# Performance work log

Hardware: AMD Instinct MI355X
Metric: run time of the kernel (lower is better)

Reference implementation:

```python
import jax, jax.numpy as jnp
import numpy as np

BATCH_SIZE = 512
NUM_ID = 64
FEAT_DIMS = 512
GROUP = BATCH_SIZE // NUM_ID


def setup_inputs() -> dict:
    key = jax.random.key(0)
    k1, k2 = jax.random.split(key)
    f_s = jax.random.normal(k1, (BATCH_SIZE, FEAT_DIMS), dtype=jnp.float32)
    f_t = jax.random.normal(k2, (BATCH_SIZE, FEAT_DIMS), dtype=jnp.float32)
    return {"f_s": f_s, "f_t": f_t}


def reference(f_s, f_t):
    B, g, n_id = BATCH_SIZE, GROUP, NUM_ID
    # all-pairs similarity: (B, B)
    sim_all = f_s @ f_t.T
    # sim_diff[i, j, k] = sim_all[i, k] - sim_all[i, j]  -> (B, B, B)
    sim_diff = sim_all[:, None, :] - sim_all[:, :, None]
    mask = 1.0 - jnp.eye(B, dtype=sim_all.dtype)  # over (j, k)
    sim_sg = jax.nn.relu(sim_diff) * mask[None, :, :]
    sim_all_rk = jnp.sum(sim_sg, axis=-1) + 1.0  # (B, B)

    # per-class positive similarities
    xs = f_s.reshape(n_id, g, FEAT_DIMS)
    xt = f_t.reshape(n_id, g, FEAT_DIMS)
    sim_pos = jnp.einsum('nid,njd->nij', xs, xt)  # (n_id, g, g)
    # sim_pos_diff[n, i, j, k] = sim_pos[n, i, k] - sim_pos[n, i, j]
    sim_pos_diff = sim_pos[:, :, None, :] - sim_pos[:, :, :, None]
    pos_mask = 1.0 - jnp.eye(g, dtype=sim_pos.dtype)  # over (j, k)
    sim_pos_sg = jax.nn.relu(sim_pos_diff) * pos_mask[None, None, :, :]
    sim_pos_rk = jnp.sum(sim_pos_sg, axis=-1) + 1.0  # (n_id, g, g)

    # block-diagonal (per-id) slices of sim_all_rk: (n_id, g, g)
    blocks = sim_all_rk.reshape(n_id, g, n_id, g)
    idx = jnp.arange(n_id)
    diag_blocks = blocks[idx, :, idx, :]  # (n_id, g, g)

    ap = jnp.sum(sim_pos_rk / diag_blocks) / g / B
    return 1.0 - ap
```

## Files before the change

### kernel.cpp

```cpp
#include <hip/hip_runtime.h>

typedef __attribute__((ext_vector_type(8))) short bf16x8;
typedef __attribute__((ext_vector_type(4))) float f32x4;

#define NB 512
#define FD 512
#define PLANE (NB * FD)

__device__ __forceinline__ ushort f2bf(float x) {
    uint u = __builtin_bit_cast(uint, x);
    return (ushort)((u + 0x7FFFu + ((u >> 16) & 1u)) >> 16);
}
__device__ __forceinline__ float bf2f(ushort h) {
    uint u = ((uint)h) << 16;
    return __builtin_bit_cast(float, u);
}

__global__ __launch_bounds__(256)
void k_split(const float* __restrict__ fs, const float* __restrict__ ft,
             ushort* __restrict__ planes, float* __restrict__ out1)
{
    const int t = blockIdx.x * 256 + threadIdx.x;
    if (t == 0) out1[0] = 1.0f;
    const int mat = t >> 16;
    const int i4  = t & 65535;
    const float4 v = ((const float4*)(mat ? ft : fs))[i4];

    ushort4 hi, lo;
    hi.x = f2bf(v.x); lo.x = f2bf(v.x - bf2f(hi.x));
    hi.y = f2bf(v.y); lo.y = f2bf(v.y - bf2f(hi.y));
    hi.z = f2bf(v.z); lo.z = f2bf(v.z - bf2f(hi.z));
    hi.w = f2bf(v.w); lo.w = f2bf(v.w - bf2f(hi.w));

    ushort4* hp = (ushort4*)(planes + (size_t)mat * 2 * PLANE);
    ushort4* lp = (ushort4*)(planes + (size_t)mat * 2 * PLANE + PLANE);
    hp[i4] = hi;
    lp[i4] = lo;
}

__global__ __launch_bounds__(64)
void k_mm(const ushort* __restrict__ planes, float* __restrict__ sim)
{
    const int l   = threadIdx.x;
    const int bid = blockIdx.x;
    const int tr  = (bid >> 4) * 32;
    const int tc  = (bid & 15) * 32;
    const int r0  = l & 15;
    const int kg  = (l >> 4) * 8;

    const ushort* fsh = planes;
    const ushort* fsl = planes + PLANE;
    const ushort* fth = planes + 2 * PLANE;
    const ushort* ftl = planes + 3 * PLANE;

    const ushort* pa0h = fsh + (size_t)(tr + r0)      * FD + kg;
    const ushort* pa1h = fsh + (size_t)(tr + r0 + 16) * FD + kg;
    const ushort* pa0l = fsl + (size_t)(tr + r0)      * FD + kg;
    const ushort* pa1l = fsl + (size_t)(tr + r0 + 16) * FD + kg;
    const ushort* pb0h = fth + (size_t)(tc + r0)      * FD + kg;
    const ushort* pb1h = fth + (size_t)(tc + r0 + 16) * FD + kg;
    const ushort* pb0l = ftl + (size_t)(tc + r0)      * FD + kg;
    const ushort* pb1l = ftl + (size_t)(tc + r0 + 16) * FD + kg;

    f32x4 acc[2][2];
    #pragma unroll
    for (int i = 0; i < 2; ++i)
        #pragma unroll
        for (int j = 0; j < 2; ++j) acc[i][j] = (f32x4){0.f, 0.f, 0.f, 0.f};

    #pragma unroll 4
    for (int k = 0; k < FD; k += 32) {
        const bf16x8 a0h = *(const bf16x8*)(pa0h + k);
        const bf16x8 a1h = *(const bf16x8*)(pa1h + k);
        const bf16x8 a0l = *(const bf16x8*)(pa0l + k);
        const bf16x8 a1l = *(const bf16x8*)(pa1l + k);
        const bf16x8 b0h = *(const bf16x8*)(pb0h + k);
        const bf16x8 b1h = *(const bf16x8*)(pb1h + k);
        const bf16x8 b0l = *(const bf16x8*)(pb0l + k);
        const bf16x8 b1l = *(const bf16x8*)(pb1l + k);

        acc[0][0] = __builtin_amdgcn_mfma_f32_16x16x32_bf16(a0h, b0h, acc[0][0], 0, 0, 0);
        acc[0][0] = __builtin_amdgcn_mfma_f32_16x16x32_bf16(a0h, b0l, acc[0][0], 0, 0, 0);
        acc[0][0] = __builtin_amdgcn_mfma_f32_16x16x32_bf16(a0l, b0h, acc[0][0], 0, 0, 0);
        acc[0][1] = __builtin_amdgcn_mfma_f32_16x16x32_bf16(a0h, b1h, acc[0][1], 0, 0, 0);
        acc[0][1] = __builtin_amdgcn_mfma_f32_16x16x32_bf16(a0h, b1l, acc[0][1], 0, 0, 0);
        acc[0][1] = __builtin_amdgcn_mfma_f32_16x16x32_bf16(a0l, b1h, acc[0][1], 0, 0, 0);
        acc[1][0] = __builtin_amdgcn_mfma_f32_16x16x32_bf16(a1h, b0h, acc[1][0], 0, 0, 0);
        acc[1][0] = __builtin_amdgcn_mfma_f32_16x16x32_bf16(a1h, b0l, acc[1][0], 0, 0, 0);
        acc[1][0] = __builtin_amdgcn_mfma_f32_16x16x32_bf16(a1l, b0h, acc[1][0], 0, 0, 0);
        acc[1][1] = __builtin_amdgcn_mfma_f32_16x16x32_bf16(a1h, b1h, acc[1][1], 0, 0, 0);
        acc[1][1] = __builtin_amdgcn_mfma_f32_16x16x32_bf16(a1h, b1l, acc[1][1], 0, 0, 0);
        acc[1][1] = __builtin_amdgcn_mfma_f32_16x16x32_bf16(a1l, b1h, acc[1][1], 0, 0, 0);
    }

    const int rbase = (l >> 4) * 4;
    #pragma unroll
    for (int mh = 0; mh < 2; ++mh)
        #pragma unroll
        for (int j = 0; j < 4; ++j) {
            const int row = tr + mh * 16 + rbase + j;
            sim[(size_t)row * NB + tc + r0]      = acc[mh][0][j];
            sim[(size_t)row * NB + tc + 16 + r0] = acc[mh][1][j];
        }
}

__global__ __launch_bounds__(512)
void k_rank(const float* __restrict__ sim, float* __restrict__ out1)
{
    __shared__ float part[8];
    const int w = threadIdx.x >> 6;
    const int l = threadIdx.x & 63;
    const int n = blockIdx.x;
    const int b = n * 8 + w;

    const float* p = sim + (size_t)b * NB + 8 * l;
    const float4 u = *(const float4*)(p);
    const float4 v = *(const float4*)(p + 4);
    float r[8] = {u.x, u.y, u.z, u.w, v.x, v.y, v.z, v.w};

    float s[8];
    #pragma unroll
    for (int q = 0; q < 8; ++q) s[q] = __shfl(r[q], n);

    float a[8];
    #pragma unroll
    for (int q = 0; q < 8; ++q) a[q] = 0.f;
    #pragma unroll
    for (int q = 0; q < 8; ++q)
        #pragma unroll
        for (int jj = 0; jj < 8; ++jj)
            a[q] += fmaxf(r[jj] - s[q], 0.f);

    #pragma unroll
    for (int off = 1; off < 64; off <<= 1)
        #pragma unroll
        for (int q = 0; q < 8; ++q)
            a[q] += __shfl_xor(a[q], off);

    float contrib = 0.f;
    if (l < 8) {
        float rp = 1.f;
        #pragma unroll
        for (int k = 0; k < 8; ++k) rp += fmaxf(s[k] - s[l], 0.f);
        contrib = rp / (1.f + a[l]);
    }
    contrib += __shfl_xor(contrib, 1);
    contrib += __shfl_xor(contrib, 2);
    contrib += __shfl_xor(contrib, 4);
    if (l == 0) part[w] = contrib;
    __syncthreads();

    if (threadIdx.x == 0) {
        float t = 0.f;
        #pragma unroll
        for (int i = 0; i < 8; ++i) t += part[i];
        atomicAdd(out1, -t * (1.f / (8.f * NB)));
    }
}

extern "C" void kernel_launch(void* const* d_in, const int* in_sizes, int n_in,
                              void* d_out, int out_size, void* d_ws, size_t ws_size,
                              hipStream_t stream)
{
    const float* fs = (const float*)d_in[0];
    const float* ft = (const float*)d_in[1];
    float* out = (float*)d_out;

    ushort* planes = (ushort*)d_ws;
    float*  sim    = (float*)((char*)d_ws + 4ull * PLANE * sizeof(ushort));

    k_split<<<dim3(512), dim3(256), 0, stream>>>(fs, ft, planes, out);
    k_mm   <<<dim3(256), dim3(64),  0, stream>>>(planes, sim);
    k_rank <<<dim3(64),  dim3(512), 0, stream>>>(sim, out);
}
```

Measured before the change: 70.24 us.

## Split matmul K dimension across four blocks and sum partials in rank kernel

The matmul now splits the 512-long reduction into four chunks, launching four times as many single-wave blocks. Each writes a partial similarity slice, and the rank kernel sums the four slices when loading its rows. This targets the low occupancy of the original 256-block launch on a large GPU, where each wave ran a long serial MFMA chain. The cost is four times the intermediate write and read traffic, plus a larger workspace that must fit in ws_size.

```diff
diff --git a/kernel.cpp b/kernel.cpp
--- a/kernel.cpp
+++ b/kernel.cpp
@@ -6,6 +6,8 @@
 #define NB 512
 #define FD 512
 #define PLANE (NB * FD)
+#define KSPLIT 4
+#define KCH (FD / KSPLIT)
 
 __device__ __forceinline__ ushort f2bf(float x) {
     uint u = __builtin_bit_cast(uint, x);
@@ -39,14 +41,16 @@
 }
 
 __global__ __launch_bounds__(64)
-void k_mm(const ushort* __restrict__ planes, float* __restrict__ sim)
+void k_mm(const ushort* __restrict__ planes, float* __restrict__ simsl)
 {
-    const int l   = threadIdx.x;
-    const int bid = blockIdx.x;
-    const int tr  = (bid >> 4) * 32;
-    const int tc  = (bid & 15) * 32;
-    const int r0  = l & 15;
-    const int kg  = (l >> 4) * 8;
+    const int l    = threadIdx.x;
+    const int bid  = blockIdx.x;
+    const int ks   = bid >> 8;
+    const int tile = bid & 255;
+    const int tr   = (tile >> 4) * 32;
+    const int tc   = (tile & 15) * 32;
+    const int r0   = l & 15;
+    const int kg   = ks * KCH + (l >> 4) * 8;
 
     const ushort* fsh = planes;
     const ushort* fsl = planes + PLANE;
@@ -68,8 +72,8 @@
         #pragma unroll
         for (int j = 0; j < 2; ++j) acc[i][j] = (f32x4){0.f, 0.f, 0.f, 0.f};
 
-    #pragma unroll 4
-    for (int k = 0; k < FD; k += 32) {
+    #pragma unroll
+    for (int k = 0; k < KCH; k += 32) {
         const bf16x8 a0h = *(const bf16x8*)(pa0h + k);
         const bf16x8 a1h = *(const bf16x8*)(pa1h + k);
         const bf16x8 a0l = *(const bf16x8*)(pa0l + k);
@@ -93,19 +97,20 @@
         acc[1][1] = __builtin_amdgcn_mfma_f32_16x16x32_bf16(a1l, b1h, acc[1][1], 0, 0, 0);
     }
 
+    float* dst = simsl + (size_t)ks * NB * NB;
     const int rbase = (l >> 4) * 4;
     #pragma unroll
     for (int mh = 0; mh < 2; ++mh)
         #pragma unroll
         for (int j = 0; j < 4; ++j) {
             const int row = tr + mh * 16 + rbase + j;
-            sim[(size_t)row * NB + tc + r0]      = acc[mh][0][j];
-            sim[(size_t)row * NB + tc + 16 + r0] = acc[mh][1][j];
+            dst[(size_t)row * NB + tc + r0]      = acc[mh][0][j];
+            dst[(size_t)row * NB + tc + 16 + r0] = acc[mh][1][j];
         }
 }
 
 __global__ __launch_bounds__(512)
-void k_rank(const float* __restrict__ sim, float* __restrict__ out1)
+void k_rank(const float* __restrict__ simsl, float* __restrict__ out1)
 {
     __shared__ float part[8];
     const int w = threadIdx.x >> 6;
@@ -113,10 +118,17 @@
     const int n = blockIdx.x;
     const int b = n * 8 + w;
 
-    const float* p = sim + (size_t)b * NB + 8 * l;
-    const float4 u = *(const float4*)(p);
-    const float4 v = *(const float4*)(p + 4);
-    float r[8] = {u.x, u.y, u.z, u.w, v.x, v.y, v.z, v.w};
+    float r[8];
+    #pragma unroll
+    for (int q = 0; q < 8; ++q) r[q] = 0.f;
+    #pragma unroll
+    for (int ks = 0; ks < KSPLIT; ++ks) {
+        const float* p = simsl + (size_t)ks * NB * NB + (size_t)b * NB + 8 * l;
+        const float4 u = *(const float4*)(p);
+        const float4 v = *(const float4*)(p + 4);
+        r[0] += u.x; r[1] += u.y; r[2] += u.z; r[3] += u.w;
+        r[4] += v.x; r[5] += v.y; r[6] += v.z; r[7] += v.w;
+    }
 
     float s[8];
     #pragma unroll
@@ -167,9 +179,9 @@
     float* out = (float*)d_out;
 
     ushort* planes = (ushort*)d_ws;
-    float*  sim    = (float*)((char*)d_ws + 4ull * PLANE * sizeof(ushort));
+    float*  simsl  = (float*)((char*)d_ws + 4ull * PLANE * sizeof(ushort));
 
-    k_split<<<dim3(512), dim3(256), 0, stream>>>(fs, ft, planes, out);
-    k_mm   <<<dim3(256), dim3(64),  0, stream>>>(planes, sim);
-    k_rank <<<dim3(64),  dim3(512), 0, stream>>>(sim, out);
+    k_split<<<dim3(512),  dim3(256), 0, stream>>>(fs, ft, planes, out);
+    k_mm   <<<dim3(1024), dim3(64),  0, stream>>>(planes, simsl);
+    k_rank <<<dim3(64),   dim3(512), 0, stream>>>(simsl, out);
 }
```

Result: faster. 67.78 us (-3.5%).
